# Performance work log

Hardware: AMD Instinct MI355X
Metric: run time of the kernel (lower is better)

## Reference

```python
import jax, jax.numpy as jnp
import numpy as np

N = 50000            # nodes (cells)
E_RAND = 1_600_000   # random edges; self loops appended -> E = E_RAND + N
DIMS = [(512, 384), (384, 256), (256, 128)]  # (in, hidden) per encoder stage
OUT = 128


def setup_inputs() -> dict:
    key = jax.random.key(0)
    ks = jax.random.split(key, 16)
    features = jax.random.normal(ks[0], (N, DIMS[0][0]), dtype=jnp.float32)
    src = jax.random.randint(ks[1], (E_RAND,), 0, N, dtype=jnp.int32)
    dst = jax.random.randint(ks[2], (E_RAND,), 0, N, dtype=jnp.int32)
    loops = jnp.arange(N, dtype=jnp.int32)  # dgl.add_self_loop
    src = jnp.concatenate([src, loops])
    dst = jnp.concatenate([dst, loops])
    inp = {"features": features, "src": src, "dst": dst}
    i = 3
    for s, (din, dout) in enumerate(DIMS):
        inp[f"sage_w{s}"] = jax.random.normal(ks[i], (dout, din), jnp.float32) / np.sqrt(din); i += 1
        inp[f"sage_b{s}"] = jnp.zeros((dout,), jnp.float32)
        inp[f"gc_w{s}"] = jax.random.normal(ks[i], (dout, dout), jnp.float32) / np.sqrt(dout); i += 1
        inp[f"gc_b{s}"] = jnp.zeros((dout,), jnp.float32)
    inp["fc_w"] = jax.random.normal(ks[i], (OUT, DIMS[-1][1]), jnp.float32) / np.sqrt(DIMS[-1][1])
    inp["fc_b"] = jnp.zeros((OUT,), jnp.float32)
    return inp


def reference(features, src, dst,
              sage_w0, sage_b0, gc_w0, gc_b0,
              sage_w1, sage_b1, gc_w1, gc_b1,
              sage_w2, sage_b2, gc_w2, gc_b2,
              fc_w, fc_b):
    ones = jnp.ones((src.shape[0],), jnp.float32)
    in_deg = jax.ops.segment_sum(ones, dst, num_segments=N)
    out_deg = jax.ops.segment_sum(ones, src, num_segments=N)
    # GraphConv norm='both' scalers (clamp degree to >=1, as DGL does)
    inv_src = jnp.where(out_deg > 0, out_deg, 1.0) ** -0.5  # [N]
    inv_dst = jnp.where(in_deg > 0, in_deg, 1.0) ** -0.5    # [N]
    sage_den = (in_deg + 1.0)[:, None]                      # SAGE 'gcn' denominator

    def sage_gcn(h, w, b):
        # DGL SAGEConv aggregator_type='gcn': (sum_neigh + self)/(in_deg+1) -> fc_neigh
        agg = jax.ops.segment_sum(h[src], dst, num_segments=N)
        return ((agg + h) / sage_den) @ w.T + b

    def graph_conv(h, w, b):
        # DGL GraphConv norm='both': D_out^{-1/2} -> sum aggregate -> D_in^{-1/2} -> W
        hn = h * inv_src[:, None]
        agg = jax.ops.segment_sum(hn[src], dst, num_segments=N)
        return (agg * inv_dst[:, None]) @ w.T + b

    params = [(sage_w0, sage_b0, gc_w0, gc_b0),
              (sage_w1, sage_b1, gc_w1, gc_b1),
              (sage_w2, sage_b2, gc_w2, gc_b2)]
    h = features
    for sw, sb, gw, gb in params:
        h = jax.nn.relu(sage_gcn(h, sw, sb))
        h = jax.nn.relu(graph_conv(h, gw, gb))
    return h @ fc_w.T + fc_b
```

## Files before the change

kernel.cpp:

```cpp
#include <hip/hip_runtime.h>
#include <cstddef>
#include <cstdint>


typedef _Float16 h8 __attribute__((ext_vector_type(8)));
typedef _Float16 h4 __attribute__((ext_vector_type(4)));
typedef float f32x4 __attribute__((ext_vector_type(4)));


__global__ __launch_bounds__(256) void deg_kernel(
    const int* __restrict__ src, const int* __restrict__ dst,
    int* __restrict__ in_deg, int* __restrict__ out_deg, int E) {
  int e = blockIdx.x * 256 + threadIdx.x;
  if (e < E) {
    atomicAdd(&in_deg[dst[e]], 1);
    atomicAdd(&out_deg[src[e]], 1);
  }
}

__global__ __launch_bounds__(1024) void scan_kernel(
    const int* __restrict__ deg, int* __restrict__ row_ptr, int n) {
  __shared__ int buf[1024];
  __shared__ int carry_s;
  if (threadIdx.x == 0) carry_s = 0;
  __syncthreads();
  for (int base = 0; base < n; base += 1024) {
    int i = base + (int)threadIdx.x;
    int v = (i < n) ? deg[i] : 0;
    buf[threadIdx.x] = v;
    __syncthreads();
    #pragma unroll
    for (int off = 1; off < 1024; off <<= 1) {
      int t = 0;
      if ((int)threadIdx.x >= off) t = buf[threadIdx.x - off];
      __syncthreads();
      buf[threadIdx.x] += t;
      __syncthreads();
    }
    int incl  = buf[threadIdx.x];
    int carry = carry_s;
    int total = buf[1023];
    __syncthreads();
    if (i < n) row_ptr[i] = carry + incl - v;
    if (threadIdx.x == 0) carry_s = carry + total;
    __syncthreads();
  }
  if (threadIdx.x == 0) row_ptr[n] = carry_s;
}

__global__ __launch_bounds__(256) void scatter_kernel(
    const int* __restrict__ src, const int* __restrict__ dst,
    const int* __restrict__ row_ptr, int* __restrict__ cnt,
    int* __restrict__ csr, int E) {
  int e = blockIdx.x * 256 + threadIdx.x;
  if (e < E) {
    int d = dst[e];
    int pos = row_ptr[d] + atomicAdd(&cnt[d], 1);
    csr[pos] = src[e];
  }
}

__global__ __launch_bounds__(256) void scaler_kernel(
    const int* __restrict__ in_deg, const int* __restrict__ out_deg,
    float* __restrict__ inv_src, float* __restrict__ inv_dst,
    float* __restrict__ inv_den, int n) {
  int i = blockIdx.x * 256 + threadIdx.x;
  if (i < n) {
    float od = (float)out_deg[i];
    float id = (float)in_deg[i];
    inv_src[i] = rsqrtf(od > 0.f ? od : 1.0f);
    inv_dst[i] = rsqrtf(id > 0.f ? id : 1.0f);
    inv_den[i] = 1.0f / (id + 1.0f);
  }
}


__global__ __launch_bounds__(256) void cvt_kernel(
    const float* __restrict__ in, _Float16* __restrict__ out,
    long n_in, long n_pad) {
  long i = ((long)blockIdx.x * 256 + (long)threadIdx.x) * 4;
  if (i >= n_pad) return;
  float4 v = (i < n_in) ? *(const float4*)(in + i) : make_float4(0.f, 0.f, 0.f, 0.f);
  h4 h = {(_Float16)v.x, (_Float16)v.y, (_Float16)v.z, (_Float16)v.w};
  *(h4*)(out + i) = h;
}


template <typename OutT>
__global__ __launch_bounds__(256) void hgemm(
    const _Float16* __restrict__ A, const _Float16* __restrict__ W,
    OutT* __restrict__ C, int Mstore, int K, int Nc,
    const float* __restrict__ row_scale, const float* __restrict__ bias) {
  __shared__ _Float16 As[128 * 32];
  __shared__ _Float16 Bs[128 * 32];
  const int tid = threadIdx.x;
  const int bm = blockIdx.x * 128, bn = blockIdx.y * 128;
  const int wave = tid >> 6, lane = tid & 63;
  const int wm = (wave & 1) * 64, wn = (wave >> 1) * 64;
  const int lrow = lane & 15, lq = lane >> 4;

  const int r0 = tid >> 2;
  const int cc = (tid & 3) * 8;
  const _Float16* Ag = A + (size_t)(bm + r0) * K + cc;
  const _Float16* Wg = W + (size_t)(bn + r0) * K + cc;
  const size_t rs64 = (size_t)64 * K;

  f32x4 acc[4][4];
  #pragma unroll
  for (int i = 0; i < 4; ++i)
    #pragma unroll
    for (int j = 0; j < 4; ++j) acc[i][j] = (f32x4){0.f, 0.f, 0.f, 0.f};

  for (int k0 = 0; k0 < K; k0 += 32) {
    uint4 a0 = *(const uint4*)(Ag + k0);
    uint4 a1 = *(const uint4*)(Ag + rs64 + k0);
    uint4 b0 = *(const uint4*)(Wg + k0);
    uint4 b1 = *(const uint4*)(Wg + rs64 + k0);
    __syncthreads();
    *(uint4*)(As + r0 * 32 + cc) = a0;
    *(uint4*)(As + (64 + r0) * 32 + cc) = a1;
    *(uint4*)(Bs + r0 * 32 + cc) = b0;
    *(uint4*)(Bs + (64 + r0) * 32 + cc) = b1;
    __syncthreads();
    h8 af[4], bf[4];
    #pragma unroll
    for (int i = 0; i < 4; ++i)
      af[i] = *(const h8*)(As + (wm + i * 16 + lrow) * 32 + lq * 8);
    #pragma unroll
    for (int j = 0; j < 4; ++j)
      bf[j] = *(const h8*)(Bs + (wn + j * 16 + lrow) * 32 + lq * 8);
    #pragma unroll
    for (int i = 0; i < 4; ++i)
      #pragma unroll
      for (int j = 0; j < 4; ++j)
        acc[i][j] = __builtin_amdgcn_mfma_f32_16x16x32_f16(af[i], bf[j], acc[i][j], 0, 0, 0);
  }

  #pragma unroll
  for (int i = 0; i < 4; ++i) {
    #pragma unroll
    for (int r = 0; r < 4; ++r) {
      const int m = bm + wm + i * 16 + lq * 4 + r;
      if (m < Mstore) {
        const float rsc = row_scale ? row_scale[m] : 1.0f;
        OutT* crow = C + (size_t)m * Nc + bn + wn + lrow;
        #pragma unroll
        for (int j = 0; j < 4; ++j) {
          float v = acc[i][j][r] * rsc;
          if (bias) v += bias[bn + wn + j * 16 + lrow];
          crow[j * 16] = (OutT)v;
        }
      }
    }
  }
}


template <int D, bool SELF>
__global__ __launch_bounds__(256) void agg_h(
    const _Float16* __restrict__ Z, const int* __restrict__ row_ptr,
    const int* __restrict__ csr, const float* __restrict__ out_scale,
    const float* __restrict__ bias, _Float16* __restrict__ out, int n) {
  constexpr int CH = D / 8;
  constexpr int GROUP = 16;
  constexpr int NV = CH / GROUP;
  const int gid = threadIdx.x >> 4;
  const int lane = threadIdx.x & 15;
  const int node = blockIdx.x * 16 + gid;
  if (node >= n) return;

  const int rs = row_ptr[node], re = row_ptr[node + 1];

  float acc[NV][8];
  #pragma unroll
  for (int v = 0; v < NV; ++v)
    #pragma unroll
    for (int q = 0; q < 8; ++q) acc[v][q] = 0.f;

  for (int e = rs; e < re; e += GROUP) {
    int m = re - e; if (m > GROUP) m = GROUP;
    int eid = (lane < m) ? csr[e + lane] : 0;
    for (int j = 0; j < m; ++j) {
      int s = __shfl(eid, j, GROUP);
      const h8* zr = (const h8*)(Z + (size_t)s * D);
      #pragma unroll
      for (int v = 0; v < NV; ++v) {
        h8 t = zr[lane + v * GROUP];
        #pragma unroll
        for (int q = 0; q < 8; ++q) acc[v][q] += (float)t[q];
      }
    }
  }

  const float osc = out_scale[node];
  const h8* zs = (const h8*)(Z + (size_t)node * D);
  _Float16* orow = out + (size_t)node * D;
  #pragma unroll
  for (int v = 0; v < NV; ++v) {
    const int idx = lane + v * GROUP;
    if (SELF) {
      h8 t = zs[idx];
      #pragma unroll
      for (int q = 0; q < 8; ++q) acc[v][q] += (float)t[q];
    }
    h8 r;
    #pragma unroll
    for (int q = 0; q < 8; ++q) {
      float x = acc[v][q] * osc + bias[idx * 8 + q];
      r[q] = (_Float16)fmaxf(x, 0.f);
    }
    *(h8*)(orow + idx * 8) = r;
  }
}


static void launch_cvt(const float* in, _Float16* out, long n_in, long n_pad,
                       hipStream_t st) {
  long thr = n_pad / 4;
  cvt_kernel<<<(int)((thr + 255) / 256), 256, 0, st>>>(in, out, n_in, n_pad);
}

extern "C" void kernel_launch(void* const* d_in, const int* in_sizes, int n_in,
                              void* d_out, int out_size, void* d_ws, size_t ws_size,
                              hipStream_t stream) {
  const float* features = (const float*)d_in[0];
  const int*   src      = (const int*)d_in[1];
  const int*   dst      = (const int*)d_in[2];
  const float* wsrc[7] = {(const float*)d_in[3],  (const float*)d_in[5],
                          (const float*)d_in[7],  (const float*)d_in[9],
                          (const float*)d_in[11], (const float*)d_in[13],
                          (const float*)d_in[15]};
  const float* sb[3] = {(const float*)d_in[4],  (const float*)d_in[8],  (const float*)d_in[12]};
  const float* gb[3] = {(const float*)d_in[6],  (const float*)d_in[10], (const float*)d_in[14]};
  const float* fc_b  = (const float*)d_in[16];

  const int N = in_sizes[0] / 512;
  const int E = in_sizes[1];
  const int MB = (N + 127) / 128;
  const int Mpad = MB * 128;

  const int wcnt[7] = {384 * 512, 384 * 384, 256 * 384, 256 * 256,
                       128 * 256, 128 * 128, 128 * 128};

  char* ws = (char*)d_ws;
  _Float16* featH = (_Float16*)ws;
  _Float16* hA    = featH + (size_t)Mpad * 512;
  _Float16* hB    = hA + (size_t)Mpad * 384;
  _Float16* wH[7];
  {
    _Float16* p = hB + (size_t)Mpad * 384;
    for (int i = 0; i < 7; ++i) { wH[i] = p; p += wcnt[i]; }
  }
  int* csr     = (int*)(wH[6] + wcnt[6]);
  int* rp      = csr + E;
  int* in_dg   = rp + (N + 1);
  int* out_dg  = in_dg + N;
  int* cnt     = out_dg + N;
  float* inv_src = (float*)(cnt + N);
  float* inv_dst = inv_src + N;
  float* inv_den = inv_dst + N;

  size_t totw = 0; for (int i = 0; i < 7; ++i) totw += wcnt[i];
  size_t needed = ((size_t)Mpad * (512 + 384 + 384) + totw) * 2 +
                  ((size_t)E + (N + 1) + 6 * (size_t)N) * 4;
  if (ws_size < needed) return;

  (void)hipMemsetAsync(in_dg, 0, sizeof(int) * 3 * (size_t)N, stream);

  const int eb = (E + 255) / 256;
  const int nb = (N + 255) / 256;
  deg_kernel<<<eb, 256, 0, stream>>>(src, dst, in_dg, out_dg, E);
  scan_kernel<<<1, 1024, 0, stream>>>(in_dg, rp, N);
  scatter_kernel<<<eb, 256, 0, stream>>>(src, dst, rp, cnt, csr, E);
  scaler_kernel<<<nb, 256, 0, stream>>>(in_dg, out_dg, inv_src, inv_dst, inv_den, N);

  launch_cvt(features, featH, (long)N * 512, (long)Mpad * 512, stream);
  for (int i = 0; i < 7; ++i) launch_cvt(wsrc[i], wH[i], wcnt[i], wcnt[i], stream);

  const int dout[3] = {384, 256, 128};
  const _Float16* h = featH;
  int K = 512;
  for (int s = 0; s < 3; ++s) {
    const int D = dout[s];
    dim3 gg(MB, D / 128);
    const int ab = (N + 15) / 16;
    hgemm<_Float16><<<gg, 256, 0, stream>>>(h, wH[2 * s], hB, Mpad, K, D, nullptr, nullptr);
    if (D == 384)      agg_h<384, true><<<ab, 256, 0, stream>>>(hB, rp, csr, inv_den, sb[s], hA, N);
    else if (D == 256) agg_h<256, true><<<ab, 256, 0, stream>>>(hB, rp, csr, inv_den, sb[s], hA, N);
    else               agg_h<128, true><<<ab, 256, 0, stream>>>(hB, rp, csr, inv_den, sb[s], hA, N);
    hgemm<_Float16><<<gg, 256, 0, stream>>>(hA, wH[2 * s + 1], hB, Mpad, D, D, inv_src, nullptr);
    if (D == 384)      agg_h<384, false><<<ab, 256, 0, stream>>>(hB, rp, csr, inv_dst, gb[s], hA, N);
    else if (D == 256) agg_h<256, false><<<ab, 256, 0, stream>>>(hB, rp, csr, inv_dst, gb[s], hA, N);
    else               agg_h<128, false><<<ab, 256, 0, stream>>>(hB, rp, csr, inv_dst, gb[s], hA, N);
    h = hA;
    K = D;
  }
  dim3 gf(MB, 1);
  hgemm<float><<<gf, 256, 0, stream>>>(h, wH[6], (float*)d_out, N, 128, 128, nullptr, fc_b);
}
```

Measured before the change: 1.371 ms.

## Rework CSR build with multi-block scan, LDS histogram, and direct-to-LDS GEMM loads

Replaces the single-block serial scan with a three-kernel multi-block scan and records each edge's atomic slot during degree counting, so the scatter pass no longer needs a second atomic. Out-degree is computed with per-block packed 16-bit LDS histograms that are then reduced. The seven weight-conversion launches are merged into one kernel. The GEMM loads tiles straight into LDS with global_load_lds instead of going through registers. This adds kernels and depends on a bin-count limit and on reusing hB as scratch space.

```diff
diff --git a/kernel.cpp b/kernel.cpp
--- a/kernel.cpp
+++ b/kernel.cpp
@@ -7,71 +7,115 @@
 typedef _Float16 h4 __attribute__((ext_vector_type(4)));
 typedef float f32x4 __attribute__((ext_vector_type(4)));
 
+#define HB 64
+
 
 __global__ __launch_bounds__(256) void deg_kernel(
-    const int* __restrict__ src, const int* __restrict__ dst,
-    int* __restrict__ in_deg, int* __restrict__ out_deg, int E) {
+    const int* __restrict__ dst, int* __restrict__ in_deg,
+    int* __restrict__ ord, int E) {
   int e = blockIdx.x * 256 + threadIdx.x;
-  if (e < E) {
-    atomicAdd(&in_deg[dst[e]], 1);
-    atomicAdd(&out_deg[src[e]], 1);
-  }
-}
-
-__global__ __launch_bounds__(1024) void scan_kernel(
-    const int* __restrict__ deg, int* __restrict__ row_ptr, int n) {
-  __shared__ int buf[1024];
-  __shared__ int carry_s;
-  if (threadIdx.x == 0) carry_s = 0;
-  __syncthreads();
-  for (int base = 0; base < n; base += 1024) {
-    int i = base + (int)threadIdx.x;
-    int v = (i < n) ? deg[i] : 0;
-    buf[threadIdx.x] = v;
-    __syncthreads();
-    #pragma unroll
-    for (int off = 1; off < 1024; off <<= 1) {
-      int t = 0;
-      if ((int)threadIdx.x >= off) t = buf[threadIdx.x - off];
-      __syncthreads();
-      buf[threadIdx.x] += t;
-      __syncthreads();
-    }
-    int incl  = buf[threadIdx.x];
-    int carry = carry_s;
-    int total = buf[1023];
-    __syncthreads();
-    if (i < n) row_ptr[i] = carry + incl - v;
-    if (threadIdx.x == 0) carry_s = carry + total;
-    __syncthreads();
-  }
-  if (threadIdx.x == 0) row_ptr[n] = carry_s;
-}
-
-__global__ __launch_bounds__(256) void scatter_kernel(
-    const int* __restrict__ src, const int* __restrict__ dst,
-    const int* __restrict__ row_ptr, int* __restrict__ cnt,
-    int* __restrict__ csr, int E) {
-  int e = blockIdx.x * 256 + threadIdx.x;
-  if (e < E) {
-    int d = dst[e];
-    int pos = row_ptr[d] + atomicAdd(&cnt[d], 1);
-    csr[pos] = src[e];
-  }
-}
-
-__global__ __launch_bounds__(256) void scaler_kernel(
+  if (e < E) ord[e] = atomicAdd(&in_deg[dst[e]], 1);
+}
+
+__global__ __launch_bounds__(1024) void histo_out_kernel(
+    const int* __restrict__ src, uint32_t* __restrict__ H, int E, int bins2) {
+  __shared__ uint32_t hh[25088];
+  for (int i = threadIdx.x; i < bins2; i += 1024) hh[i] = 0;
+  __syncthreads();
+  const int C = (E + HB - 1) / HB;
+  const int base = blockIdx.x * C;
+  int lim = base + C; if (lim > E) lim = E;
+  for (int e = base + (int)threadIdx.x; e < lim; e += 1024) {
+    int s = src[e];
+    atomicAdd(&hh[s >> 1], 1u << ((s & 1) * 16));
+  }
+  __syncthreads();
+  uint32_t* out = H + (size_t)blockIdx.x * bins2;
+  for (int i = threadIdx.x; i < bins2; i += 1024) out[i] = hh[i];
+}
+
+__global__ __launch_bounds__(256) void reduce_out_kernel(
+    const uint32_t* __restrict__ H, int* __restrict__ out_deg,
+    int bins2, int n) {
+  int i = blockIdx.x * 256 + threadIdx.x;
+  if (i >= bins2) return;
+  uint32_t lo = 0, hi = 0;
+  for (int b = 0; b < HB; ++b) {
+    uint32_t v = H[(size_t)b * bins2 + i];
+    lo += v & 0xFFFFu;
+    hi += v >> 16;
+  }
+  out_deg[2 * i] = (int)lo;
+  if (2 * i + 1 < n) out_deg[2 * i + 1] = (int)hi;
+}
+
+
+__global__ __launch_bounds__(256) void scan_a(
+    const int* __restrict__ deg, int* __restrict__ bsum, int n) {
+  __shared__ int s[256];
+  int i = blockIdx.x * 256 + threadIdx.x;
+  s[threadIdx.x] = (i < n) ? deg[i] : 0;
+  __syncthreads();
+  #pragma unroll
+  for (int off = 128; off > 0; off >>= 1) {
+    if ((int)threadIdx.x < off) s[threadIdx.x] += s[threadIdx.x + off];
+    __syncthreads();
+  }
+  if (threadIdx.x == 0) bsum[blockIdx.x] = s[0];
+}
+
+__global__ __launch_bounds__(256) void scan_b(
+    int* __restrict__ bsum, int* __restrict__ rp, int nb, int n) {
+  __shared__ int s[256];
+  const int t = threadIdx.x;
+  int v = (t < nb) ? bsum[t] : 0;
+  s[t] = v;
+  __syncthreads();
+  #pragma unroll
+  for (int off = 1; off < 256; off <<= 1) {
+    int a = (t >= off) ? s[t - off] : 0;
+    __syncthreads();
+    s[t] += a;
+    __syncthreads();
+  }
+  bsum[256 + t] = s[t] - v;
+  if (t == 255) rp[n] = s[255];
+}
+
+__global__ __launch_bounds__(256) void scan_c(
     const int* __restrict__ in_deg, const int* __restrict__ out_deg,
+    const int* __restrict__ bsum, int* __restrict__ rp,
     float* __restrict__ inv_src, float* __restrict__ inv_dst,
     float* __restrict__ inv_den, int n) {
-  int i = blockIdx.x * 256 + threadIdx.x;
+  __shared__ int s[256];
+  const int t = threadIdx.x;
+  const int i = blockIdx.x * 256 + t;
+  int v = (i < n) ? in_deg[i] : 0;
+  s[t] = v;
+  __syncthreads();
+  #pragma unroll
+  for (int off = 1; off < 256; off <<= 1) {
+    int a = (t >= off) ? s[t - off] : 0;
+    __syncthreads();
+    s[t] += a;
+    __syncthreads();
+  }
   if (i < n) {
+    rp[i] = bsum[256 + blockIdx.x] + s[t] - v;
     float od = (float)out_deg[i];
-    float id = (float)in_deg[i];
+    float id = (float)v;
     inv_src[i] = rsqrtf(od > 0.f ? od : 1.0f);
     inv_dst[i] = rsqrtf(id > 0.f ? id : 1.0f);
     inv_den[i] = 1.0f / (id + 1.0f);
   }
+}
+
+__global__ __launch_bounds__(256) void scatter_kernel(
+    const int* __restrict__ src, const int* __restrict__ dst,
+    const int* __restrict__ rp, const int* __restrict__ ord,
+    int* __restrict__ csr, int E) {
+  int e = blockIdx.x * 256 + threadIdx.x;
+  if (e < E) csr[rp[dst[e]] + ord[e]] = src[e];
 }
 
 
@@ -83,6 +127,28 @@
   float4 v = (i < n_in) ? *(const float4*)(in + i) : make_float4(0.f, 0.f, 0.f, 0.f);
   h4 h = {(_Float16)v.x, (_Float16)v.y, (_Float16)v.z, (_Float16)v.w};
   *(h4*)(out + i) = h;
+}
+
+struct WArgs {
+  const float* s[7];
+  _Float16* d[7];
+  int n[7];
+};
+
+__global__ __launch_bounds__(256) void wcvt_kernel(WArgs a) {
+  const int w = blockIdx.y;
+  long i = ((long)blockIdx.x * 256 + (long)threadIdx.x) * 4;
+  if (i >= a.n[w]) return;
+  float4 v = *(const float4*)(a.s[w] + i);
+  h4 h = {(_Float16)v.x, (_Float16)v.y, (_Float16)v.z, (_Float16)v.w};
+  *(h4*)(a.d[w] + i) = h;
+}
+
+
+__device__ __forceinline__ void gload_lds16(const _Float16* g, _Float16* l) {
+  __builtin_amdgcn_global_load_lds(
+      (const __attribute__((address_space(1))) void*)g,
+      (__attribute__((address_space(3))) void*)l, 16, 0, 0);
 }
 
 
@@ -104,6 +170,10 @@
   const _Float16* Ag = A + (size_t)(bm + r0) * K + cc;
   const _Float16* Wg = W + (size_t)(bn + r0) * K + cc;
   const size_t rs64 = (size_t)64 * K;
+  _Float16* As0 = As + tid * 8;
+  _Float16* As1 = As + 64 * 32 + tid * 8;
+  _Float16* Bs0 = Bs + tid * 8;
+  _Float16* Bs1 = Bs + 64 * 32 + tid * 8;
 
   f32x4 acc[4][4];
   #pragma unroll
@@ -112,15 +182,11 @@
     for (int j = 0; j < 4; ++j) acc[i][j] = (f32x4){0.f, 0.f, 0.f, 0.f};
 
   for (int k0 = 0; k0 < K; k0 += 32) {
-    uint4 a0 = *(const uint4*)(Ag + k0);
-    uint4 a1 = *(const uint4*)(Ag + rs64 + k0);
-    uint4 b0 = *(const uint4*)(Wg + k0);
-    uint4 b1 = *(const uint4*)(Wg + rs64 + k0);
-    __syncthreads();
-    *(uint4*)(As + r0 * 32 + cc) = a0;
-    *(uint4*)(As + (64 + r0) * 32 + cc) = a1;
-    *(uint4*)(Bs + r0 * 32 + cc) = b0;
-    *(uint4*)(Bs + (64 + r0) * 32 + cc) = b1;
+    __syncthreads();
+    gload_lds16(Ag + k0, As0);
+    gload_lds16(Ag + rs64 + k0, As1);
+    gload_lds16(Wg + k0, Bs0);
+    gload_lds16(Wg + rs64 + k0, Bs1);
     __syncthreads();
     h8 af[4], bf[4];
     #pragma unroll
@@ -213,12 +279,6 @@
   }
 }
 
-
-static void launch_cvt(const float* in, _Float16* out, long n_in, long n_pad,
-                       hipStream_t st) {
-  long thr = n_pad / 4;
-  cvt_kernel<<<(int)((thr + 255) / 256), 256, 0, st>>>(in, out, n_in, n_pad);
-}
 
 extern "C" void kernel_launch(void* const* d_in, const int* in_sizes, int n_in,
                               void* d_out, int out_size, void* d_ws, size_t ws_size,
@@ -238,6 +298,8 @@
   const int E = in_sizes[1];
   const int MB = (N + 127) / 128;
   const int Mpad = MB * 128;
+  const int bins2 = (N + 1) / 2;
+  if (bins2 > 25088) return;
 
   const int wcnt[7] = {384 * 512, 384 * 384, 256 * 384, 256 * 256,
                        128 * 256, 128 * 128, 128 * 128};
@@ -255,27 +317,46 @@
   int* rp      = csr + E;
   int* in_dg   = rp + (N + 1);
   int* out_dg  = in_dg + N;
-  int* cnt     = out_dg + N;
-  float* inv_src = (float*)(cnt + N);
+  int* sblk    = out_dg + N;
+  float* inv_src = (float*)(sblk + N);
   float* inv_dst = inv_src + N;
   float* inv_den = inv_dst + N;
+
+  int*      ord = (int*)hB;
+  uint32_t* H64 = (uint32_t*)(ord + E);
 
   size_t totw = 0; for (int i = 0; i < 7; ++i) totw += wcnt[i];
   size_t needed = ((size_t)Mpad * (512 + 384 + 384) + totw) * 2 +
                   ((size_t)E + (N + 1) + 6 * (size_t)N) * 4;
   if (ws_size < needed) return;
 
-  (void)hipMemsetAsync(in_dg, 0, sizeof(int) * 3 * (size_t)N, stream);
+  (void)hipMemsetAsync(in_dg, 0, sizeof(int) * (size_t)N, stream);
 
   const int eb = (E + 255) / 256;
-  const int nb = (N + 255) / 256;
-  deg_kernel<<<eb, 256, 0, stream>>>(src, dst, in_dg, out_dg, E);
-  scan_kernel<<<1, 1024, 0, stream>>>(in_dg, rp, N);
-  scatter_kernel<<<eb, 256, 0, stream>>>(src, dst, rp, cnt, csr, E);
-  scaler_kernel<<<nb, 256, 0, stream>>>(in_dg, out_dg, inv_src, inv_dst, inv_den, N);
-
-  launch_cvt(features, featH, (long)N * 512, (long)Mpad * 512, stream);
-  for (int i = 0; i < 7; ++i) launch_cvt(wsrc[i], wH[i], wcnt[i], wcnt[i], stream);
+  const int nb256 = (N + 255) / 256;
+
+  deg_kernel<<<eb, 256, 0, stream>>>(dst, in_dg, ord, E);
+  histo_out_kernel<<<HB, 1024, 0, stream>>>(src, H64, E, bins2);
+  reduce_out_kernel<<<(bins2 + 255) / 256, 256, 0, stream>>>(H64, out_dg, bins2, N);
+  scan_a<<<nb256, 256, 0, stream>>>(in_dg, sblk, N);
+  scan_b<<<1, 256, 0, stream>>>(sblk, rp, nb256, N);
+  scan_c<<<nb256, 256, 0, stream>>>(in_dg, out_dg, sblk, rp,
+                                    inv_src, inv_dst, inv_den, N);
+  scatter_kernel<<<eb, 256, 0, stream>>>(src, dst, rp, ord, csr, E);
+
+  {
+    long thr = (long)Mpad * 512 / 4;
+    cvt_kernel<<<(int)((thr + 255) / 256), 256, 0, stream>>>(
+        features, featH, (long)N * 512, (long)Mpad * 512);
+    WArgs wa;
+    int maxn = 0;
+    for (int i = 0; i < 7; ++i) {
+      wa.s[i] = wsrc[i]; wa.d[i] = wH[i]; wa.n[i] = wcnt[i];
+      if (wcnt[i] > maxn) maxn = wcnt[i];
+    }
+    dim3 wg((maxn / 4 + 255) / 256, 7);
+    wcvt_kernel<<<wg, 256, 0, stream>>>(wa);
+  }
 
   const int dout[3] = {384, 256, 128};
   const _Float16* h = featH;
```

Measured after the change: 1.192 ms. 13.0% less time.
